# Performance work log

Hardware: AMD Instinct MI355X
Metric: run time of the kernel (lower is better)

The kernel has to match this reference:

```python
import jax, jax.numpy as jnp
import numpy as np

B, S, D, H, L = 32, 512, 256, 8, 3
HD = D // H
FFN = D // 2
SCALE_BASE = 512.0
EPS = 1e-5


def _gammas():
    return (1.0 - jnp.exp(jnp.linspace(np.log(1.0 / 32.0), np.log(1.0 / 512.0), H))).astype(jnp.float32)


def _xpos(x, downscale):
    # x: [..., S, hd]; XPOS rotary embedding with exponential length scaling
    s, hd = x.shape[-2], x.shape[-1]
    half = hd // 2
    scale = (jnp.arange(0, hd, 2, dtype=jnp.float32) + 0.4 * hd) / (1.4 * hd)  # [half]
    power = jnp.arange(s, dtype=jnp.float32)[:, None] / SCALE_BASE
    sm = scale[None, :] ** power  # [S, half]
    if downscale:
        sm = 1.0 / sm
    inv_freq = 1.0 / (10000.0 ** (jnp.arange(half, dtype=jnp.float32) / half))
    ang = jnp.arange(s, dtype=jnp.float32)[:, None] * inv_freq[None, :]  # [S, half]
    sin = jnp.repeat(jnp.sin(ang) * sm, 2, axis=-1)  # duplicate_interleave -> [S, hd]
    cos = jnp.repeat(jnp.cos(ang) * sm, 2, axis=-1)
    x1, x2 = x[..., ::2], x[..., 1::2]
    rot = jnp.stack((-x2, x1), axis=-1).reshape(x.shape)  # rotate_every_two
    return x * cos + rot * sin


def _layer_norm(x, w, b):
    mu = x.mean(-1, keepdims=True)
    var = ((x - mu) ** 2).mean(-1, keepdims=True)
    return (x - mu) / jnp.sqrt(var + EPS) * w + b


def _msr(X, WQ, WK, WV, WG, WO, gn_w, gn_b):
    # Multi-scale retention, parallel form. X: [B,S,D]; WQ/WK/WV: [H,D,HD]
    b, s, _ = X.shape
    Q = _xpos(jnp.einsum('bsd,hde->bhse', X, WQ), False)
    K = _xpos(jnp.einsum('bsd,hde->bhse', X, WK), True)
    V = jnp.einsum('bsd,hde->bhse', X, WV)
    n = jnp.arange(s)
    delta = (n[:, None] - n[None, :]).astype(jnp.float32)
    mask = n[:, None] >= n[None, :]
    g = _gammas()
    Dm = jnp.where(mask[None], g[:, None, None] ** delta[None], 0.0)  # [H,S,S]
    scores = jnp.einsum('bhse,bhte->bhst', Q, K) * Dm[None]  # [B,H,S,S]
    Y = jnp.einsum('bhst,bhte->bhse', scores, V)  # [B,H,S,HD]
    Y = jnp.moveaxis(Y, 1, 2)  # [B,S,H,HD] (= concat heads)
    # GroupNorm(heads, v_dim): normalize per (token, head) group
    mu = Y.mean(-1, keepdims=True)
    var = ((Y - mu) ** 2).mean(-1, keepdims=True)
    Yn = ((Y - mu) / jnp.sqrt(var + EPS)).reshape(b, s, D) * gn_w + gn_b
    G = X @ WG
    return (G * jax.nn.sigmoid(G) * Yn) @ WO


def setup_inputs() -> dict:
    key = jax.random.key(0)
    ks = jax.random.split(key, 10)
    inp = {
        'v': jax.random.randint(ks[0], (B, S), 0, 65, dtype=jnp.int64),
        'emb': jax.random.normal(ks[1], (65, D), dtype=jnp.float32),
        'WQ': jax.random.normal(ks[2], (L, H, D, HD), dtype=jnp.float32) / D,
        'WK': jax.random.normal(ks[3], (L, H, D, HD), dtype=jnp.float32) / D,
        'WV': jax.random.normal(ks[4], (L, H, D, HD), dtype=jnp.float32) / D,
        'WG': jax.random.normal(ks[5], (L, D, D), dtype=jnp.float32) / D,
        'WO': jax.random.normal(ks[6], (L, D, D), dtype=jnp.float32) / D,
        'gn_w': jnp.ones((L, D), jnp.float32),
        'gn_b': jnp.zeros((L, D), jnp.float32),
        'ln1_w': jnp.ones((L, D), jnp.float32),
        'ln1_b': jnp.zeros((L, D), jnp.float32),
        'ln2_w': jnp.ones((L, D), jnp.float32),
        'ln2_b': jnp.zeros((L, D), jnp.float32),
        'w1': jax.random.normal(ks[7], (L, D, FFN), dtype=jnp.float32) * (1.0 / np.sqrt(D)),
        'b1': jnp.zeros((L, FFN), jnp.float32),
        'w2': jax.random.normal(ks[8], (L, FFN, D), dtype=jnp.float32) * (1.0 / np.sqrt(FFN)),
        'b2': jnp.zeros((L, D), jnp.float32),
    }
    return inp


def reference(v, emb, WQ, WK, WV, WG, WO, gn_w, gn_b, ln1_w, ln1_b, ln2_w, ln2_b, w1, b1, w2, b2):
    emb = emb.at[0].set(0.0)  # padding_idx=0
    X = jax.nn.relu(emb[v])  # [B,S,D]
    for i in range(L):
        Y = _msr(_layer_norm(X, ln1_w[i], ln1_b[i]), WQ[i], WK[i], WV[i], WG[i], WO[i], gn_w[i], gn_b[i]) + X
        h = jax.nn.gelu(_layer_norm(Y, ln2_w[i], ln2_b[i]) @ w1[i] + b1[i], approximate=False)
        X = h @ w2[i] + b2[i] + Y
    return X
```

## Files before the change

kernel.cpp:

```cpp
#include <hip/hip_runtime.h>
#include <hip/hip_bf16.h>
#include <math.h>

#define BB 32
#define SS 512
#define DD 256
#define HH 8
#define HDIM 32
#define FFNN 128
#define NROWS (BB*SS)
#define NELEM (NROWS*DD)

using bf16 = __hip_bfloat16;
typedef __attribute__((ext_vector_type(8))) short short8;
typedef __attribute__((ext_vector_type(4))) short short4v;
typedef __attribute__((ext_vector_type(4))) float floatx4;
typedef unsigned int uint_al __attribute__((may_alias));

static __device__ __forceinline__ float bf2f(bf16 x) { return __bfloat162float(x); }
static __device__ __forceinline__ bf16  f2bf(float x) { return __float2bfloat16(x); }
static __device__ __forceinline__ short f2bfs(float x) {
    bf16 b = __float2bfloat16(x);
    return __builtin_bit_cast(short, b);
}

static __device__ __forceinline__ unsigned int cvtpk(float a, float b) {
    unsigned int r;
    asm("v_cvt_pk_bf16_f32 %0, %1, %2" : "=v"(r) : "v"(a), "v"(b));
    return r;
}
static __device__ __forceinline__ short4v mk4(unsigned int a, unsigned int b) {
    union { unsigned int u[2]; short4v s; } t;
    t.u[0] = a; t.u[1] = b;
    return t.s;
}
static __device__ __forceinline__ floatx4 mfma16(short4v a, short4v b, floatx4 c) {
#if __has_builtin(__builtin_amdgcn_mfma_f32_16x16x16bf16_1k)
    return __builtin_amdgcn_mfma_f32_16x16x16bf16_1k(a, b, c, 0, 0, 0);
#else
    asm("v_mfma_f32_16x16x16_bf16 %0, %1, %2, %0" : "+v"(c) : "v"(a), "v"(b));
    return c;
#endif
}

static __device__ __forceinline__ void gld_lds16(const void* g, void* l) {
    __builtin_amdgcn_global_load_lds(
        (const __attribute__((address_space(1))) void*)g,
        (__attribute__((address_space(3))) void*)l, 16, 0, 0);
}

__global__ __launch_bounds__(256) void detect_v(const int* __restrict__ v, int* __restrict__ flag) {
    int i = blockIdx.x * 256 + threadIdx.x;
    if (v[2 * i + 1] != 0) atomicOr(flag, 1);
}

#define NQKVG (3*1024*256)
#define NWO   (3*256*256)
#define NW1   (3*128*256)
#define NW2   (3*256*128)
#define NXPT  (512*16)
#define NSETUP (NQKVG+NWO+NW1+NW2+NXPT)
__global__ __launch_bounds__(256) void setup_pack(const float* __restrict__ WQ, const float* __restrict__ WK,
                                                  const float* __restrict__ WV, const float* __restrict__ WG,
                                                  const float* __restrict__ WO, const float* __restrict__ w1,
                                                  const float* __restrict__ w2,
                                                  bf16* __restrict__ dQ, bf16* __restrict__ dO,
                                                  bf16* __restrict__ d1, bf16* __restrict__ d2,
                                                  float4* __restrict__ xpt, int* __restrict__ flag) {
    int idx = blockIdx.x * 256 + threadIdx.x;
    if (idx == 0) *flag = 0;
    if (idx < NQKVG) {
        int k = idx & 255, n = (idx >> 8) & 1023, l = idx >> 18;
        int seg = n >> 8, n8 = n & 255;
        float val;
        if (seg < 3) {
            const float* W = (seg == 0) ? WQ : (seg == 1) ? WK : WV;
            int h = n8 >> 5, e = n8 & 31;
            val = W[(((size_t)l * 8 + h) * 256 + k) * 32 + e];
        } else {
            val = WG[(size_t)l * 65536 + k * 256 + n8];
        }
        dQ[((size_t)l * 1024 + n) * 256 + k] = f2bf(val);
    } else if (idx < NQKVG + NWO) {
        int i = idx - NQKVG;
        int k = i & 255, n = (i >> 8) & 255, l = i >> 16;
        dO[((size_t)l * 256 + n) * 256 + k] = f2bf(WO[(size_t)l * 65536 + k * 256 + n]);
    } else if (idx < NQKVG + NWO + NW1) {
        int i = idx - NQKVG - NWO;
        int k = i & 255, n = (i >> 8) & 127, l = i >> 15;
        d1[((size_t)l * 128 + n) * 256 + k] = f2bf(w1[(size_t)l * 32768 + k * 128 + n]);
    } else if (idx < NQKVG + NWO + NW1 + NW2) {
        int i = idx - NQKVG - NWO - NW1;
        int k = i & 127, n = (i >> 7) & 255, l = i >> 15;
        d2[((size_t)l * 256 + n) * 128 + k] = f2bf(w2[(size_t)l * 32768 + k * 256 + n]);
    } else {
        int i = idx - NQKVG - NWO - NW1 - NW2;
        int jf = i & 15, s = i >> 4;
        float base = (2.0f * jf + 12.8f) / 44.8f;
        float sm = powf(base, (float)s * (1.0f / 512.0f));
        float ang = (float)s * powf(10000.0f, -(float)jf / 16.0f);
        float sn, cs;
        sincosf(ang, &sn, &cs);
        xpt[i] = float4{cs * sm, sn * sm, cs / sm, sn / sm};
    }
}

__global__ __launch_bounds__(256) void embed_ln_kernel(const int* __restrict__ v,
                                                       const float* __restrict__ emb,
                                                       const int* __restrict__ flag,
                                                       const float* __restrict__ w,
                                                       const float* __restrict__ b,
                                                       float* __restrict__ X,
                                                       short* __restrict__ Xn) {
    __shared__ float p1[4], p2[4], st[2];
    const int d = threadIdx.x;
    const int wid = threadIdx.x >> 6;
    const int is32 = *flag;
    const float wd = w[d], bd = b[d];
    for (int it = 0; it < 8; ++it) {
        int row = blockIdx.x * 8 + it;
        int tok = is32 ? v[row] : v[2 * row];
        float x = 0.0f;
        if (tok != 0) {
            x = emb[tok * DD + d];
            x = x > 0.0f ? x : 0.0f;
        }
        X[(size_t)row * DD + d] = x;
        float s1 = x, s2 = x * x;
        #pragma unroll
        for (int off = 1; off < 64; off <<= 1) {
            s1 += __shfl_xor(s1, off);
            s2 += __shfl_xor(s2, off);
        }
        if ((threadIdx.x & 63) == 0) { p1[wid] = s1; p2[wid] = s2; }
        __syncthreads();
        if (threadIdx.x == 0) {
            float t1 = p1[0] + p1[1] + p1[2] + p1[3];
            float t2 = p2[0] + p2[1] + p2[2] + p2[3];
            float mu = t1 * (1.0f / DD);
            float var = t2 * (1.0f / DD) - mu * mu;
            st[0] = mu; st[1] = rsqrtf(var + 1e-5f);
        }
        __syncthreads();
        Xn[(size_t)row * DD + d] = f2bfs((x - st[0]) * st[1] * wd + bd);
    }
}

__global__ __launch_bounds__(256) void qkvg_gemm(const short* __restrict__ A,
                                                 const short* __restrict__ Bp,
                                                 const float4* __restrict__ xpt,
                                                 bf16* __restrict__ C) {
    __shared__ __align__(16) short Als[16 * 512];
    __shared__ __align__(16) short Bls[16 * 512];
    const int tid = threadIdx.x;
    const int wave = tid >> 6, lane = tid & 63, lo = lane & 15, quad = lane >> 4;
    const int wm = wave >> 1, wn = wave & 1;
    const int row0 = blockIdx.x * 128, col0 = blockIdx.y * 128;

    floatx4 acc[4][4];
    #pragma unroll
    for (int i = 0; i < 4; ++i)
        #pragma unroll
        for (int j = 0; j < 4; ++j) acc[i][j] = floatx4{0.f, 0.f, 0.f, 0.f};

    for (int k0 = 0; k0 < 256; k0 += 64) {
        #pragma unroll
        for (int t = 0; t < 4; ++t) {
            int grp = (wm * 4 + t) * 2 + wn;
            const short* ga = A + (size_t)(row0 + (wm * 4 + t) * 16 + lo) * 256
                            + k0 + (wn * 4 + quad) * 8;
            gld_lds16(ga, &Als[grp * 512]);
        }
        #pragma unroll
        for (int t = 0; t < 4; ++t) {
            int grp = (wn * 4 + t) * 2 + wm;
            const short* gb = Bp + (size_t)(col0 + (wn * 4 + t) * 16 + lo) * 256
                            + k0 + (wm * 4 + quad) * 8;
            gld_lds16(gb, &Bls[grp * 512]);
        }
        __syncthreads();
        #pragma unroll
        for (int kkgrp = 0; kkgrp < 2; ++kkgrp) {
            short8 af[4], bfr[4];
            #pragma unroll
            for (int t = 0; t < 4; ++t)
                af[t] = *(const short8*)(&Als[((wm * 4 + t) * 2 + kkgrp) * 512 + lane * 8]);
            #pragma unroll
            for (int t = 0; t < 4; ++t)
                bfr[t] = *(const short8*)(&Bls[((wn * 4 + t) * 2 + kkgrp) * 512 + lane * 8]);
            #pragma unroll
            for (int ti = 0; ti < 4; ++ti)
                #pragma unroll
                for (int tj = 0; tj < 4; ++tj)
                    acc[ti][tj] = __builtin_amdgcn_mfma_f32_16x16x32_bf16(af[ti], bfr[tj], acc[ti][tj], 0, 0, 0);
        }
        __syncthreads();
    }

    #pragma unroll
    for (int ti = 0; ti < 4; ++ti) {
        #pragma unroll
        for (int tj = 0; tj < 4; ++tj) {
            int colb = col0 + (wn * 4 + tj) * 16 + lo;
            int seg = colb >> 8;
            #pragma unroll
            for (int r = 0; r < 4; ++r) {
                int row = row0 + (wm * 4 + ti) * 16 + quad * 4 + r;
                float v = acc[ti][tj][r];
                if (seg < 2) {
                    int s = row & (SS - 1);
                    int jf = (colb & 31) >> 1;
                    float4 t = xpt[s * 16 + jf];
                    float cs = (seg == 0) ? t.x : t.z;
                    float sn = (seg == 0) ? t.y : t.w;
                    float p = __shfl_xor(v, 1);
                    v = (lo & 1) ? (v * cs + p * sn) : (v * cs - p * sn);
                }
                C[(size_t)row * 1024 + colb] = f2bf(v);
            }
        }
    }
}

#define TSTR 264
#define HSTR 136
#define VSTR 42
template<int DOLN>
__global__ __launch_bounds__(512) void ret_wo_ffn(const bf16* __restrict__ QKVG,
                                                  const float* __restrict__ gnw,
                                                  const float* __restrict__ gnb,
                                                  const short* __restrict__ Wo,
                                                  const short* __restrict__ W1p,
                                                  const float* __restrict__ b1,
                                                  const short* __restrict__ W2p,
                                                  const float* __restrict__ b2,
                                                  float* __restrict__ X,
                                                  const float* __restrict__ ln2w,
                                                  const float* __restrict__ ln2b,
                                                  const float* __restrict__ ln1w,
                                                  const float* __restrict__ ln1b,
                                                  short* __restrict__ Xn) {
    __shared__ __align__(16) short Vt[8][32 * VSTR];
    __shared__ __align__(16) short Tn[32 * TSTR];
    __shared__ __align__(16) short Hf[32 * HSTR];
    __shared__ float Ssum[32][8], Ssq[32][8];
    const int tid = threadIdx.x;
    const int wave = tid >> 6, lane = tid & 63, lo = lane & 15, quad = lane >> 4;
    const int blk = blockIdx.x;
    const int xcd = blk & 7;
    const int slot = blk >> 3;
    int qi, bbl;
    if (slot < 32) { qi = slot & 15; bbl = slot >> 4; }
    else { qi = 15 - (slot & 15); bbl = 2 + ((slot - 32) >> 4); }
    const int bb = (xcd << 2) | bbl;
    const int q0 = qi * 32;
    const int row0 = bb * SS + q0;
    const int h = wave;
    const int kq = quad * 8;

    const size_t base = (size_t)bb * SS * 1024;
    const short* QKVGs = (const short*)QKVG;
    const float la0 = -3.46573590280f, la1 = -6.23832462504f;
    float gamma = 1.0f - expf(la0 + (float)h * (la1 - la0) / 7.0f);
    float lg2 = log2f(gamma);
    float g16i = exp2f(-16.0f * lg2);
    float g16p = exp2f(16.0f * lg2);
    float gi32 = exp2f(-32.0f * lg2);
    float wq[4], wq16[4], wqB[4];
    #pragma unroll
    for (int r = 0; r < 4; ++r) {
        wq[r]   = exp2f((float)(lo - 4 * quad - r) * lg2);
        wq16[r] = wq[r] * g16i;
        wqB[r]  = wq[r] * g16p;
    }
    float c = exp2f((float)q0 * lg2);

    short8 qfA = *(const short8*)(QKVGs + base + (size_t)(q0 + lo) * 1024 + h * HDIM + kq);
    short8 qfB = *(const short8*)(QKVGs + base + (size_t)(q0 + 16 + lo) * 1024 + h * HDIM + kq);

    floatx4 oA0 = {0,0,0,0}, oA1 = {0,0,0,0}, oB0 = {0,0,0,0}, oB1 = {0,0,0,0};
    short* Vw = Vt[wave];
    const int nch = qi + 1;

    for (int ch = 0; ch < nch; ++ch) {
        const int t0 = ch * 32;
        const short* Kb = QKVGs + base + 256 + h * HDIM + kq;
        short8 kf0 = *(const short8*)(Kb + (size_t)(t0 + lo) * 1024);
        short8 kf1 = *(const short8*)(Kb + (size_t)(t0 + 16 + lo) * 1024);
        {
            const int vr = lane >> 2, dcol = (lane & 3) * 8;
            const short* Vg = QKVGs + base + 512 + h * HDIM + dcol;
            uint4 u1 = *(const uint4*)(Vg + (size_t)(t0 + vr) * 1024);
            uint4 u2 = *(const uint4*)(Vg + (size_t)(t0 + 16 + vr) * 1024);
            uint_al* W1 = (uint_al*)(Vw + vr * VSTR + dcol);
            uint_al* W2 = (uint_al*)(Vw + (16 + vr) * VSTR + dcol);
            W1[0] = u1.x; W1[1] = u1.y; W1[2] = u1.z; W1[3] = u1.w;
            W2[0] = u2.x; W2[1] = u2.y; W2[2] = u2.z; W2[3] = u2.w;
        }
        const floatx4 z = {0,0,0,0};
        __builtin_amdgcn_s_setprio(1);
        floatx4 sA0 = __builtin_amdgcn_mfma_f32_16x16x32_bf16(kf0, qfA, z, 0, 0, 0);
        floatx4 sA1 = __builtin_amdgcn_mfma_f32_16x16x32_bf16(kf1, qfA, z, 0, 0, 0);
        floatx4 sB0 = __builtin_amdgcn_mfma_f32_16x16x32_bf16(kf0, qfB, z, 0, 0, 0);
        floatx4 sB1 = __builtin_amdgcn_mfma_f32_16x16x32_bf16(kf1, qfB, z, 0, 0, 0);
        __builtin_amdgcn_s_setprio(0);

        float m0[4], m1[4], mB[4];
        #pragma unroll
        for (int r = 0; r < 4; ++r) {
            m0[r] = c * wq[r];
            m1[r] = c * wq16[r];
            mB[r] = c * wqB[r];
        }
        if (ch == qi) {
            #pragma unroll
            for (int r = 0; r < 4; ++r) {
                if (lo < 4 * quad + r) m0[r] = 0.0f;
                m1[r] = 0.0f;
            }
        }
        c *= gi32;

        unsigned int pa0 = cvtpk(sA0[0] * m0[0], sA0[1] * m0[1]);
        unsigned int pa1 = cvtpk(sA0[2] * m0[2], sA0[3] * m0[3]);
        unsigned int pa2 = cvtpk(sA1[0] * m1[0], sA1[1] * m1[1]);
        unsigned int pa3 = cvtpk(sA1[2] * m1[2], sA1[3] * m1[3]);
        unsigned int pb0 = cvtpk(sB0[0] * mB[0], sB0[1] * mB[1]);
        unsigned int pb1 = cvtpk(sB0[2] * mB[2], sB0[3] * mB[3]);
        unsigned int pb2 = cvtpk(sB1[0] * m0[0], sB1[1] * m0[1]);
        unsigned int pb3 = cvtpk(sB1[2] * m0[2], sB1[3] * m0[3]);
        short4v pA0 = mk4(pa0, pa1), pA1 = mk4(pa2, pa3);
        short4v pB0 = mk4(pb0, pb1), pB1 = mk4(pb2, pb3);

        short4v v00, v01, v10, v11;
        #pragma unroll
        for (int j = 0; j < 4; ++j) {
            v00[j] = Vw[(4 * quad + j) * VSTR + lo];
            v01[j] = Vw[(16 + 4 * quad + j) * VSTR + lo];
            v10[j] = Vw[(4 * quad + j) * VSTR + 16 + lo];
            v11[j] = Vw[(16 + 4 * quad + j) * VSTR + 16 + lo];
        }
        __builtin_amdgcn_s_setprio(1);
        oA0 = mfma16(pA0, v00, oA0);
        oA0 = mfma16(pA1, v01, oA0);
        oA1 = mfma16(pA0, v10, oA1);
        oA1 = mfma16(pA1, v11, oA1);
        oB0 = mfma16(pB0, v00, oB0);
        oB0 = mfma16(pB1, v01, oB0);
        oB1 = mfma16(pB0, v10, oB1);
        oB1 = mfma16(pB1, v11, oB1);
        __builtin_amdgcn_s_setprio(0);
    }

    {
        float gw0 = gnw[h * HDIM + lo], gw1 = gnw[h * HDIM + 16 + lo];
        float gb0 = gnb[h * HDIM + lo], gb1 = gnb[h * HDIM + 16 + lo];
        #pragma unroll
        for (int sub = 0; sub < 2; ++sub) {
            floatx4 o0 = sub ? oB0 : oA0;
            floatx4 o1 = sub ? oB1 : oA1;
            #pragma unroll
            for (int r = 0; r < 4; ++r) {
                float y0 = o0[r], y1 = o1[r];
                float s = y0 + y1, ss = y0 * y0 + y1 * y1;
                #pragma unroll
                for (int off = 1; off < 16; off <<= 1) {
                    s  += __shfl_xor(s, off);
                    ss += __shfl_xor(ss, off);
                }
                float mu = s * (1.0f / HDIM);
                float var = ss * (1.0f / HDIM) - mu * mu;
                float rstd = rsqrtf(var + 1e-5f);
                int rl = sub * 16 + quad * 4 + r;
                size_t rowb = base + (size_t)(q0 + rl) * 1024;
                float g0 = bf2f(QKVG[rowb + 768 + h * HDIM + lo]);
                float g1 = bf2f(QKVG[rowb + 768 + h * HDIM + 16 + lo]);
                float t0v = g0 / (1.0f + expf(-g0)) * ((y0 - mu) * rstd * gw0 + gb0);
                float t1v = g1 / (1.0f + expf(-g1)) * ((y1 - mu) * rstd * gw1 + gb1);
                Tn[rl * TSTR + h * HDIM + lo]      = f2bfs(t0v);
                Tn[rl * TSTR + h * HDIM + 16 + lo] = f2bfs(t1v);
            }
        }
    }
    __syncthreads();

    floatx4 acc[2][2];
    #pragma unroll
    for (int i = 0; i < 2; ++i) { acc[i][0] = floatx4{0,0,0,0}; acc[i][1] = floatx4{0,0,0,0}; }
    for (int k0 = 0; k0 < 256; k0 += 64) {
        #pragma unroll
        for (int kk = 0; kk < 2; ++kk) {
            const int kof = k0 + kk * 32 + kq;
            short8 af[2], bfr[2];
            #pragma unroll
            for (int t = 0; t < 2; ++t)
                af[t] = *(const short8*)(&Tn[(t * 16 + lo) * TSTR + kof]);
            #pragma unroll
            for (int t = 0; t < 2; ++t)
                bfr[t] = *(const short8*)(Wo + (size_t)(wave * 32 + t * 16 + lo) * 256 + kof);
            #pragma unroll
            for (int ti = 0; ti < 2; ++ti)
                #pragma unroll
                for (int tj = 0; tj < 2; ++tj)
                    acc[ti][tj] = __builtin_amdgcn_mfma_f32_16x16x32_bf16(af[ti], bfr[tj], acc[ti][tj], 0, 0, 0);
        }
    }

    float vv[2][2][4];
    #pragma unroll
    for (int ti = 0; ti < 2; ++ti)
        #pragma unroll
        for (int tj = 0; tj < 2; ++tj) {
            int colb = wave * 32 + tj * 16 + lo;
            #pragma unroll
            for (int r = 0; r < 4; ++r) {
                int row = row0 + ti * 16 + quad * 4 + r;
                vv[ti][tj][r] = acc[ti][tj][r] + X[(size_t)row * DD + colb];
            }
        }
    #pragma unroll
    for (int ti = 0; ti < 2; ++ti)
        #pragma unroll
        for (int r = 0; r < 4; ++r) {
            float s1 = 0.f, s2 = 0.f;
            #pragma unroll
            for (int tj = 0; tj < 2; ++tj) {
                float v = vv[ti][tj][r];
                s1 += v; s2 += v * v;
            }
            #pragma unroll
            for (int off = 1; off < 16; off <<= 1) {
                s1 += __shfl_xor(s1, off);
                s2 += __shfl_xor(s2, off);
            }
            if (lo == 0) {
                int rl = ti * 16 + quad * 4 + r;
                Ssum[rl][wave] = s1;
                Ssq[rl][wave] = s2;
            }
        }
    __syncthreads();
    #pragma unroll
    for (int ti = 0; ti < 2; ++ti)
        #pragma unroll
        for (int r = 0; r < 4; ++r) {
            int rl = ti * 16 + quad * 4 + r;
            float t1 = 0.f, t2 = 0.f;
            #pragma unroll
            for (int w8 = 0; w8 < 8; ++w8) { t1 += Ssum[rl][w8]; t2 += Ssq[rl][w8]; }
            float mu = t1 * (1.0f / DD);
            float var = t2 * (1.0f / DD) - mu * mu;
            float rs = rsqrtf(var + 1e-5f);
            #pragma unroll
            for (int tj = 0; tj < 2; ++tj) {
                int colb = wave * 32 + tj * 16 + lo;
                Tn[rl * TSTR + colb] =
                    f2bfs((vv[ti][tj][r] - mu) * rs * ln2w[colb] + ln2b[colb]);
            }
        }
    __syncthreads();

    floatx4 a1[2];
    a1[0] = floatx4{0,0,0,0}; a1[1] = floatx4{0,0,0,0};
    for (int k0 = 0; k0 < 256; k0 += 64) {
        #pragma unroll
        for (int kk = 0; kk < 2; ++kk) {
            const int kof = k0 + kk * 32 + kq;
            short8 af[2], bfr;
            #pragma unroll
            for (int t = 0; t < 2; ++t)
                af[t] = *(const short8*)(&Tn[(t * 16 + lo) * TSTR + kof]);
            bfr = *(const short8*)(W1p + (size_t)(wave * 16 + lo) * 256 + kof);
            #pragma unroll
            for (int ti = 0; ti < 2; ++ti)
                a1[ti] = __builtin_amdgcn_mfma_f32_16x16x32_bf16(af[ti], bfr, a1[ti], 0, 0, 0);
        }
    }
    {
        int colb = wave * 16 + lo;
        float bs = b1[colb];
        #pragma unroll
        for (int ti = 0; ti < 2; ++ti)
            #pragma unroll
            for (int r = 0; r < 4; ++r) {
                int rl = ti * 16 + quad * 4 + r;
                float v = a1[ti][r] + bs;
                v = 0.5f * v * (1.0f + erff(v * 0.70710678118f));
                Hf[rl * HSTR + colb] = f2bfs(v);
            }
    }
    __syncthreads();

    floatx4 a2[2][2];
    #pragma unroll
    for (int i = 0; i < 2; ++i) { a2[i][0] = floatx4{0,0,0,0}; a2[i][1] = floatx4{0,0,0,0}; }
    for (int k0 = 0; k0 < 128; k0 += 64) {
        #pragma unroll
        for (int kk = 0; kk < 2; ++kk) {
            const int kof = k0 + kk * 32 + kq;
            short8 af[2], bfr[2];
            #pragma unroll
            for (int t = 0; t < 2; ++t)
                af[t] = *(const short8*)(&Hf[(t * 16 + lo) * HSTR + kof]);
            #pragma unroll
            for (int t = 0; t < 2; ++t)
                bfr[t] = *(const short8*)(W2p + (size_t)(wave * 32 + t * 16 + lo) * 128 + kof);
            #pragma unroll
            for (int ti = 0; ti < 2; ++ti)
                #pragma unroll
                for (int tj = 0; tj < 2; ++tj)
                    a2[ti][tj] = __builtin_amdgcn_mfma_f32_16x16x32_bf16(af[ti], bfr[tj], a2[ti][tj], 0, 0, 0);
        }
    }

    #pragma unroll
    for (int ti = 0; ti < 2; ++ti)
        #pragma unroll
        for (int tj = 0; tj < 2; ++tj) {
            int colb = wave * 32 + tj * 16 + lo;
            float bs = b2[colb];
            #pragma unroll
            for (int r = 0; r < 4; ++r) {
                int row = row0 + ti * 16 + quad * 4 + r;
                float v = a2[ti][tj][r] + bs + vv[ti][tj][r];
                X[(size_t)row * DD + colb] = v;
                vv[ti][tj][r] = v;
            }
        }
    if (!DOLN) return;
    #pragma unroll
    for (int ti = 0; ti < 2; ++ti)
        #pragma unroll
        for (int r = 0; r < 4; ++r) {
            float s1 = 0.f, s2 = 0.f;
            #pragma unroll
            for (int tj = 0; tj < 2; ++tj) {
                float v = vv[ti][tj][r];
                s1 += v; s2 += v * v;
            }
            #pragma unroll
            for (int off = 1; off < 16; off <<= 1) {
                s1 += __shfl_xor(s1, off);
                s2 += __shfl_xor(s2, off);
            }
            if (lo == 0) {
                int rl = ti * 16 + quad * 4 + r;
                Ssum[rl][wave] = s1;
                Ssq[rl][wave] = s2;
            }
        }
    __syncthreads();
    #pragma unroll
    for (int ti = 0; ti < 2; ++ti)
        #pragma unroll
        for (int r = 0; r < 4; ++r) {
            int rl = ti * 16 + quad * 4 + r;
            float t1 = 0.f, t2 = 0.f;
            #pragma unroll
            for (int w8 = 0; w8 < 8; ++w8) { t1 += Ssum[rl][w8]; t2 += Ssq[rl][w8]; }
            float mu = t1 * (1.0f / DD);
            float var = t2 * (1.0f / DD) - mu * mu;
            float rs = rsqrtf(var + 1e-5f);
            int row = row0 + rl;
            #pragma unroll
            for (int tj = 0; tj < 2; ++tj) {
                int colb = wave * 32 + tj * 16 + lo;
                Xn[(size_t)row * DD + colb] =
                    f2bfs((vv[ti][tj][r] - mu) * rs * ln1w[colb] + ln1b[colb]);
            }
        }
}

extern "C" void kernel_launch(void* const* d_in, const int* in_sizes, int n_in,
                              void* d_out, int out_size, void* d_ws, size_t ws_size,
                              hipStream_t stream) {
    const int*   v    = (const int*)d_in[0];
    const float* emb  = (const float*)d_in[1];
    const float* WQ   = (const float*)d_in[2];
    const float* WK   = (const float*)d_in[3];
    const float* WV   = (const float*)d_in[4];
    const float* WG   = (const float*)d_in[5];
    const float* WO   = (const float*)d_in[6];
    const float* gn_w = (const float*)d_in[7];
    const float* gn_b = (const float*)d_in[8];
    const float* ln1w = (const float*)d_in[9];
    const float* ln1b = (const float*)d_in[10];
    const float* ln2w = (const float*)d_in[11];
    const float* ln2b = (const float*)d_in[12];
    const float* w1   = (const float*)d_in[13];
    const float* b1   = (const float*)d_in[14];
    const float* w2   = (const float*)d_in[15];
    const float* b2   = (const float*)d_in[16];

    float* X = (float*)d_out;

    float* base  = (float*)d_ws;
    int*   flag  = (int*)base;
    short* Xn    = (short*)(base + 16);
    bf16*  QKVG  = (bf16*)(Xn + (size_t)NROWS * 256);
    bf16*  WqkvgP = QKVG + (size_t)NROWS * 1024;
    bf16*  WoP   = WqkvgP + 3 * 1024 * 256;
    bf16*  W1P   = WoP + 3 * 256 * 256;
    bf16*  W2P   = W1P + 3 * 128 * 256;
    float4* xpt  = (float4*)(W2P + 3 * 256 * 128);

    setup_pack<<<NSETUP / 256, 256, 0, stream>>>(WQ, WK, WV, WG, WO, w1, w2,
                                                 WqkvgP, WoP, W1P, W2P, xpt, flag);
    detect_v<<<32, 256, 0, stream>>>(v, flag);
    embed_ln_kernel<<<NROWS / 8, 256, 0, stream>>>(v, emb, flag, ln1w, ln1b, X, Xn);

    for (int i = 0; i < 3; ++i) {
        qkvg_gemm<<<dim3(128, 8), 256, 0, stream>>>(Xn,
                                                    (const short*)(WqkvgP + (size_t)i * 1024 * 256),
                                                    xpt, QKVG);
        if (i < 2)
            ret_wo_ffn<1><<<512, 512, 0, stream>>>(QKVG, gn_w + i * DD, gn_b + i * DD,
                                                   (const short*)(WoP + (size_t)i * 256 * 256),
                                                   (const short*)(W1P + (size_t)i * 128 * 256),
                                                   b1 + i * FFNN,
                                                   (const short*)(W2P + (size_t)i * 256 * 128),
                                                   b2 + i * DD, X,
                                                   ln2w + i * DD, ln2b + i * DD,
                                                   ln1w + (i + 1) * DD, ln1b + (i + 1) * DD, Xn);
        else
            ret_wo_ffn<0><<<512, 512, 0, stream>>>(QKVG, gn_w + i * DD, gn_b + i * DD,
                                                   (const short*)(WoP + (size_t)i * 256 * 256),
                                                   (const short*)(W1P + (size_t)i * 128 * 256),
                                                   b1 + i * FFNN,
                                                   (const short*)(W2P + (size_t)i * 256 * 128),
                                                   b2 + i * DD, X,
                                                   ln2w + i * DD, ln2b + i * DD,
                                                   nullptr, nullptr, nullptr);
    }
}
```

Measured before the change: 347.8 us.

## Halve query tile to 16 rows and double grid in fused retention kernel

```diff
diff --git a/kernel.cpp b/kernel.cpp
--- a/kernel.cpp
+++ b/kernel.cpp
@@ -240,23 +240,24 @@
                                                   const float* __restrict__ ln1w,
                                                   const float* __restrict__ ln1b,
                                                   short* __restrict__ Xn) {
-    __shared__ __align__(16) short Vt[8][32 * VSTR];
-    __shared__ __align__(16) short Tn[32 * TSTR];
-    __shared__ __align__(16) short Hf[32 * HSTR];
-    __shared__ float Ssum[32][8], Ssq[32][8];
+    __shared__ __align__(16) short Tn[16 * TSTR];
+    __shared__ __align__(16) short Ubuf[8 * 16 * VSTR];
     const int tid = threadIdx.x;
     const int wave = tid >> 6, lane = tid & 63, lo = lane & 15, quad = lane >> 4;
     const int blk = blockIdx.x;
     const int xcd = blk & 7;
     const int slot = blk >> 3;
-    int qi, bbl;
-    if (slot < 32) { qi = slot & 15; bbl = slot >> 4; }
-    else { qi = 15 - (slot & 15); bbl = 2 + ((slot - 32) >> 4); }
-    const int bb = (xcd << 2) | bbl;
-    const int q0 = qi * 32;
+    const int g = slot >> 5, rr = slot & 31;
+    const int qt = (g & 1) ? (31 - rr) : rr;
+    const int bb = (xcd << 2) | g;
+    const int q0 = qt * 16;
     const int row0 = bb * SS + q0;
     const int h = wave;
     const int kq = quad * 8;
+
+    short* Hf = Ubuf;
+    float* Ssum = (float*)(Ubuf + 16 * HSTR);
+    float* Ssq  = Ssum + 16 * 8;
 
     const size_t base = (size_t)bb * SS * 1024;
     const short* QKVGs = (const short*)QKVG;
@@ -264,91 +265,56 @@
     float gamma = 1.0f - expf(la0 + (float)h * (la1 - la0) / 7.0f);
     float lg2 = log2f(gamma);
     float g16i = exp2f(-16.0f * lg2);
-    float g16p = exp2f(16.0f * lg2);
-    float gi32 = exp2f(-32.0f * lg2);
-    float wq[4], wq16[4], wqB[4];
-    #pragma unroll
-    for (int r = 0; r < 4; ++r) {
-        wq[r]   = exp2f((float)(lo - 4 * quad - r) * lg2);
-        wq16[r] = wq[r] * g16i;
-        wqB[r]  = wq[r] * g16p;
-    }
+    float wq[4];
+    #pragma unroll
+    for (int r = 0; r < 4; ++r)
+        wq[r] = exp2f((float)(lo - 4 * quad - r) * lg2);
     float c = exp2f((float)q0 * lg2);
 
-    short8 qfA = *(const short8*)(QKVGs + base + (size_t)(q0 + lo) * 1024 + h * HDIM + kq);
-    short8 qfB = *(const short8*)(QKVGs + base + (size_t)(q0 + 16 + lo) * 1024 + h * HDIM + kq);
-
-    floatx4 oA0 = {0,0,0,0}, oA1 = {0,0,0,0}, oB0 = {0,0,0,0}, oB1 = {0,0,0,0};
-    short* Vw = Vt[wave];
-    const int nch = qi + 1;
-
-    for (int ch = 0; ch < nch; ++ch) {
-        const int t0 = ch * 32;
-        const short* Kb = QKVGs + base + 256 + h * HDIM + kq;
-        short8 kf0 = *(const short8*)(Kb + (size_t)(t0 + lo) * 1024);
-        short8 kf1 = *(const short8*)(Kb + (size_t)(t0 + 16 + lo) * 1024);
+    short8 qf = *(const short8*)(QKVGs + base + (size_t)(q0 + lo) * 1024 + h * HDIM + kq);
+
+    floatx4 o0 = {0,0,0,0}, o1 = {0,0,0,0};
+    short* Vw = Ubuf + wave * (16 * VSTR);
+    const int nch = qt + 1;
+    const short* Kb = QKVGs + base + 256 + h * HDIM + kq;
+    const int vr = lane >> 2, dcol = (lane & 3) * 8;
+    const short* Vg = QKVGs + base + 512 + h * HDIM + dcol;
+
+    for (int ct = 0; ct < nch; ++ct) {
+        const int t0 = ct * 16;
+        short8 kf = *(const short8*)(Kb + (size_t)(t0 + lo) * 1024);
         {
-            const int vr = lane >> 2, dcol = (lane & 3) * 8;
-            const short* Vg = QKVGs + base + 512 + h * HDIM + dcol;
             uint4 u1 = *(const uint4*)(Vg + (size_t)(t0 + vr) * 1024);
-            uint4 u2 = *(const uint4*)(Vg + (size_t)(t0 + 16 + vr) * 1024);
             uint_al* W1 = (uint_al*)(Vw + vr * VSTR + dcol);
-            uint_al* W2 = (uint_al*)(Vw + (16 + vr) * VSTR + dcol);
             W1[0] = u1.x; W1[1] = u1.y; W1[2] = u1.z; W1[3] = u1.w;
-            W2[0] = u2.x; W2[1] = u2.y; W2[2] = u2.z; W2[3] = u2.w;
         }
         const floatx4 z = {0,0,0,0};
         __builtin_amdgcn_s_setprio(1);
-        floatx4 sA0 = __builtin_amdgcn_mfma_f32_16x16x32_bf16(kf0, qfA, z, 0, 0, 0);
-        floatx4 sA1 = __builtin_amdgcn_mfma_f32_16x16x32_bf16(kf1, qfA, z, 0, 0, 0);
-        floatx4 sB0 = __builtin_amdgcn_mfma_f32_16x16x32_bf16(kf0, qfB, z, 0, 0, 0);
-        floatx4 sB1 = __builtin_amdgcn_mfma_f32_16x16x32_bf16(kf1, qfB, z, 0, 0, 0);
+        floatx4 sA = __builtin_amdgcn_mfma_f32_16x16x32_bf16(kf, qf, z, 0, 0, 0);
         __builtin_amdgcn_s_setprio(0);
 
-        float m0[4], m1[4], mB[4];
-        #pragma unroll
-        for (int r = 0; r < 4; ++r) {
-            m0[r] = c * wq[r];
-            m1[r] = c * wq16[r];
-            mB[r] = c * wqB[r];
-        }
-        if (ch == qi) {
-            #pragma unroll
-            for (int r = 0; r < 4; ++r) {
+        float m0[4];
+        #pragma unroll
+        for (int r = 0; r < 4; ++r) m0[r] = c * wq[r];
+        if (ct == qt) {
+            #pragma unroll
+            for (int r = 0; r < 4; ++r)
                 if (lo < 4 * quad + r) m0[r] = 0.0f;
-                m1[r] = 0.0f;
-            }
-        }
-        c *= gi32;
-
-        unsigned int pa0 = cvtpk(sA0[0] * m0[0], sA0[1] * m0[1]);
-        unsigned int pa1 = cvtpk(sA0[2] * m0[2], sA0[3] * m0[3]);
-        unsigned int pa2 = cvtpk(sA1[0] * m1[0], sA1[1] * m1[1]);
-        unsigned int pa3 = cvtpk(sA1[2] * m1[2], sA1[3] * m1[3]);
-        unsigned int pb0 = cvtpk(sB0[0] * mB[0], sB0[1] * mB[1]);
-        unsigned int pb1 = cvtpk(sB0[2] * mB[2], sB0[3] * mB[3]);
-        unsigned int pb2 = cvtpk(sB1[0] * m0[0], sB1[1] * m0[1]);
-        unsigned int pb3 = cvtpk(sB1[2] * m0[2], sB1[3] * m0[3]);
-        short4v pA0 = mk4(pa0, pa1), pA1 = mk4(pa2, pa3);
-        short4v pB0 = mk4(pb0, pb1), pB1 = mk4(pb2, pb3);
-
-        short4v v00, v01, v10, v11;
+        }
+        c *= g16i;
+
+        short4v pA = mk4(cvtpk(sA[0] * m0[0], sA[1] * m0[1]),
+                         cvtpk(sA[2] * m0[2], sA[3] * m0[3]));
+
+        short4v v0, v1;
         #pragma unroll
         for (int j = 0; j < 4; ++j) {
-            v00[j] = Vw[(4 * quad + j) * VSTR + lo];
-            v01[j] = Vw[(16 + 4 * quad + j) * VSTR + lo];
-            v10[j] = Vw[(4 * quad + j) * VSTR + 16 + lo];
-            v11[j] = Vw[(16 + 4 * quad + j) * VSTR + 16 + lo];
+            v0[j] = Vw[(4 * quad + j) * VSTR + lo];
+            v1[j] = Vw[(4 * quad + j) * VSTR + 16 + lo];
         }
         __builtin_amdgcn_s_setprio(1);
-        oA0 = mfma16(pA0, v00, oA0);
-        oA0 = mfma16(pA1, v01, oA0);
-        oA1 = mfma16(pA0, v10, oA1);
-        oA1 = mfma16(pA1, v11, oA1);
-        oB0 = mfma16(pB0, v00, oB0);
-        oB0 = mfma16(pB1, v01, oB0);
-        oB1 = mfma16(pB0, v10, oB1);
-        oB1 = mfma16(pB1, v11, oB1);
+        o0 = mfma16(pA, v0, o0);
+        o1 = mfma16(pA, v1, o1);
         __builtin_amdgcn_s_setprio(0);
     }
 
@@ -356,219 +322,173 @@
         float gw0 = gnw[h * HDIM + lo], gw1 = gnw[h * HDIM + 16 + lo];
         float gb0 = gnb[h * HDIM + lo], gb1 = gnb[h * HDIM + 16 + lo];
         #pragma unroll
-        for (int sub = 0; sub < 2; ++sub) {
-            floatx4 o0 = sub ? oB0 : oA0;
-            floatx4 o1 = sub ? oB1 : oA1;
-            #pragma unroll
-            for (int r = 0; r < 4; ++r) {
-                float y0 = o0[r], y1 = o1[r];
-                float s = y0 + y1, ss = y0 * y0 + y1 * y1;
-                #pragma unroll
-                for (int off = 1; off < 16; off <<= 1) {
-                    s  += __shfl_xor(s, off);
-                    ss += __shfl_xor(ss, off);
-                }
-                float mu = s * (1.0f / HDIM);
-                float var = ss * (1.0f / HDIM) - mu * mu;
-                float rstd = rsqrtf(var + 1e-5f);
-                int rl = sub * 16 + quad * 4 + r;
-                size_t rowb = base + (size_t)(q0 + rl) * 1024;
-                float g0 = bf2f(QKVG[rowb + 768 + h * HDIM + lo]);
-                float g1 = bf2f(QKVG[rowb + 768 + h * HDIM + 16 + lo]);
-                float t0v = g0 / (1.0f + expf(-g0)) * ((y0 - mu) * rstd * gw0 + gb0);
-                float t1v = g1 / (1.0f + expf(-g1)) * ((y1 - mu) * rstd * gw1 + gb1);
-                Tn[rl * TSTR + h * HDIM + lo]      = f2bfs(t0v);
-                Tn[rl * TSTR + h * HDIM + 16 + lo] = f2bfs(t1v);
+        for (int r = 0; r < 4; ++r) {
+            float y0 = o0[r], y1 = o1[r];
+            float s = y0 + y1, ss = y0 * y0 + y1 * y1;
+            #pragma unroll
+            for (int off = 1; off < 16; off <<= 1) {
+                s  += __shfl_xor(s, off);
+                ss += __shfl_xor(ss, off);
             }
+            float mu = s * (1.0f / HDIM);
+            float var = ss * (1.0f / HDIM) - mu * mu;
+            float rstd = rsqrtf(var + 1e-5f);
+            int rl = quad * 4 + r;
+            size_t rowb = base + (size_t)(q0 + rl) * 1024;
+            float g0 = bf2f(QKVG[rowb + 768 + h * HDIM + lo]);
+            float g1 = bf2f(QKVG[rowb + 768 + h * HDIM + 16 + lo]);
+            float t0v = g0 / (1.0f + expf(-g0)) * ((y0 - mu) * rstd * gw0 + gb0);
+            float t1v = g1 / (1.0f + expf(-g1)) * ((y1 - mu) * rstd * gw1 + gb1);
+            Tn[rl * TSTR + h * HDIM + lo]      = f2bfs(t0v);
+            Tn[rl * TSTR + h * HDIM + 16 + lo] = f2bfs(t1v);
         }
     }
     __syncthreads();
 
-    floatx4 acc[2][2];
-    #pragma unroll
-    for (int i = 0; i < 2; ++i) { acc[i][0] = floatx4{0,0,0,0}; acc[i][1] = floatx4{0,0,0,0}; }
+    floatx4 acc[2];
+    acc[0] = floatx4{0,0,0,0}; acc[1] = floatx4{0,0,0,0};
     for (int k0 = 0; k0 < 256; k0 += 64) {
         #pragma unroll
         for (int kk = 0; kk < 2; ++kk) {
             const int kof = k0 + kk * 32 + kq;
-            short8 af[2], bfr[2];
-            #pragma unroll
-            for (int t = 0; t < 2; ++t)
-                af[t] = *(const short8*)(&Tn[(t * 16 + lo) * TSTR + kof]);
-            #pragma unroll
-            for (int t = 0; t < 2; ++t)
-                bfr[t] = *(const short8*)(Wo + (size_t)(wave * 32 + t * 16 + lo) * 256 + kof);
-            #pragma unroll
-            for (int ti = 0; ti < 2; ++ti)
-                #pragma unroll
-                for (int tj = 0; tj < 2; ++tj)
-                    acc[ti][tj] = __builtin_amdgcn_mfma_f32_16x16x32_bf16(af[ti], bfr[tj], acc[ti][tj], 0, 0, 0);
-        }
-    }
-
-    float vv[2][2][4];
-    #pragma unroll
-    for (int ti = 0; ti < 2; ++ti)
+            short8 af = *(const short8*)(&Tn[lo * TSTR + kof]);
+            #pragma unroll
+            for (int tj = 0; tj < 2; ++tj) {
+                short8 bfr = *(const short8*)(Wo + (size_t)(wave * 32 + tj * 16 + lo) * 256 + kof);
+                acc[tj] = __builtin_amdgcn_mfma_f32_16x16x32_bf16(af, bfr, acc[tj], 0, 0, 0);
+            }
+        }
+    }
+
+    float vv[2][4];
+    #pragma unroll
+    for (int tj = 0; tj < 2; ++tj) {
+        int colb = wave * 32 + tj * 16 + lo;
+        #pragma unroll
+        for (int r = 0; r < 4; ++r) {
+            int row = row0 + quad * 4 + r;
+            vv[tj][r] = acc[tj][r] + X[(size_t)row * DD + colb];
+        }
+    }
+    #pragma unroll
+    for (int r = 0; r < 4; ++r) {
+        float s1 = vv[0][r] + vv[1][r];
+        float s2 = vv[0][r] * vv[0][r] + vv[1][r] * vv[1][r];
+        #pragma unroll
+        for (int off = 1; off < 16; off <<= 1) {
+            s1 += __shfl_xor(s1, off);
+            s2 += __shfl_xor(s2, off);
+        }
+        if (lo == 0) {
+            int rl = quad * 4 + r;
+            Ssum[rl * 8 + wave] = s1;
+            Ssq[rl * 8 + wave] = s2;
+        }
+    }
+    __syncthreads();
+    #pragma unroll
+    for (int r = 0; r < 4; ++r) {
+        int rl = quad * 4 + r;
+        float t1 = 0.f, t2 = 0.f;
+        #pragma unroll
+        for (int w8 = 0; w8 < 8; ++w8) { t1 += Ssum[rl * 8 + w8]; t2 += Ssq[rl * 8 + w8]; }
+        float mu = t1 * (1.0f / DD);
+        float var = t2 * (1.0f / DD) - mu * mu;
+        float rs = rsqrtf(var + 1e-5f);
         #pragma unroll
         for (int tj = 0; tj < 2; ++tj) {
             int colb = wave * 32 + tj * 16 + lo;
-            #pragma unroll
-            for (int r = 0; r < 4; ++r) {
-                int row = row0 + ti * 16 + quad * 4 + r;
-                vv[ti][tj][r] = acc[ti][tj][r] + X[(size_t)row * DD + colb];
-            }
-        }
-    #pragma unroll
-    for (int ti = 0; ti < 2; ++ti)
-        #pragma unroll
-        for (int r = 0; r < 4; ++r) {
-            float s1 = 0.f, s2 = 0.f;
-            #pragma unroll
-            for (int tj = 0; tj < 2; ++tj) {
-                float v = vv[ti][tj][r];
-                s1 += v; s2 += v * v;
-            }
-            #pragma unroll
-            for (int off = 1; off < 16; off <<= 1) {
-                s1 += __shfl_xor(s1, off);
-                s2 += __shfl_xor(s2, off);
-            }
-            if (lo == 0) {
-                int rl = ti * 16 + quad * 4 + r;
-                Ssum[rl][wave] = s1;
-                Ssq[rl][wave] = s2;
-            }
-        }
+            Tn[rl * TSTR + colb] =
+                f2bfs((vv[tj][r] - mu) * rs * ln2w[colb] + ln2b[colb]);
+        }
+    }
     __syncthreads();
-    #pragma unroll
-    for (int ti = 0; ti < 2; ++ti)
-        #pragma unroll
-        for (int r = 0; r < 4; ++r) {
-            int rl = ti * 16 + quad * 4 + r;
-            float t1 = 0.f, t2 = 0.f;
-            #pragma unroll
-            for (int w8 = 0; w8 < 8; ++w8) { t1 += Ssum[rl][w8]; t2 += Ssq[rl][w8]; }
-            float mu = t1 * (1.0f / DD);
-            float var = t2 * (1.0f / DD) - mu * mu;
-            float rs = rsqrtf(var + 1e-5f);
-            #pragma unroll
-            for (int tj = 0; tj < 2; ++tj) {
-                int colb = wave * 32 + tj * 16 + lo;
-                Tn[rl * TSTR + colb] =
-                    f2bfs((vv[ti][tj][r] - mu) * rs * ln2w[colb] + ln2b[colb]);
-            }
-        }
-    __syncthreads();
-
-    floatx4 a1[2];
-    a1[0] = floatx4{0,0,0,0}; a1[1] = floatx4{0,0,0,0};
+
+    floatx4 a1 = {0,0,0,0};
     for (int k0 = 0; k0 < 256; k0 += 64) {
         #pragma unroll
         for (int kk = 0; kk < 2; ++kk) {
             const int kof = k0 + kk * 32 + kq;
-            short8 af[2], bfr;
-            #pragma unroll
-            for (int t = 0; t < 2; ++t)
-                af[t] = *(const short8*)(&Tn[(t * 16 + lo) * TSTR + kof]);
-            bfr = *(const short8*)(W1p + (size_t)(wave * 16 + lo) * 256 + kof);
-            #pragma unroll
-            for (int ti = 0; ti < 2; ++ti)
-                a1[ti] = __builtin_amdgcn_mfma_f32_16x16x32_bf16(af[ti], bfr, a1[ti], 0, 0, 0);
+            short8 af = *(const short8*)(&Tn[lo * TSTR + kof]);
+            short8 bfr = *(const short8*)(W1p + (size_t)(wave * 16 + lo) * 256 + kof);
+            a1 = __builtin_amdgcn_mfma_f32_16x16x32_bf16(af, bfr, a1, 0, 0, 0);
         }
     }
     {
         int colb = wave * 16 + lo;
         float bs = b1[colb];
         #pragma unroll
-        for (int ti = 0; ti < 2; ++ti)
-            #pragma unroll
-            for (int r = 0; r < 4; ++r) {
-                int rl = ti * 16 + quad * 4 + r;
-                float v = a1[ti][r] + bs;
-                v = 0.5f * v * (1.0f + erff(v * 0.70710678118f));
-                Hf[rl * HSTR + colb] = f2bfs(v);
-            }
+        for (int r = 0; r < 4; ++r) {
+            int rl = quad * 4 + r;
+            float v = a1[r] + bs;
+            v = 0.5f * v * (1.0f + erff(v * 0.70710678118f));
+            Hf[rl * HSTR + colb] = f2bfs(v);
+        }
     }
     __syncthreads();
 
-    floatx4 a2[2][2];
-    #pragma unroll
-    for (int i = 0; i < 2; ++i) { a2[i][0] = floatx4{0,0,0,0}; a2[i][1] = floatx4{0,0,0,0}; }
+    floatx4 a2[2];
+    a2[0] = floatx4{0,0,0,0}; a2[1] = floatx4{0,0,0,0};
     for (int k0 = 0; k0 < 128; k0 += 64) {
         #pragma unroll
         for (int kk = 0; kk < 2; ++kk) {
             const int kof = k0 + kk * 32 + kq;
-            short8 af[2], bfr[2];
-            #pragma unroll
-            for (int t = 0; t < 2; ++t)
-                af[t] = *(const short8*)(&Hf[(t * 16 + lo) * HSTR + kof]);
-            #pragma unroll
-            for (int t = 0; t < 2; ++t)
-                bfr[t] = *(const short8*)(W2p + (size_t)(wave * 32 + t * 16 + lo) * 128 + kof);
-            #pragma unroll
-            for (int ti = 0; ti < 2; ++ti)
-                #pragma unroll
-                for (int tj = 0; tj < 2; ++tj)
-                    a2[ti][tj] = __builtin_amdgcn_mfma_f32_16x16x32_bf16(af[ti], bfr[tj], a2[ti][tj], 0, 0, 0);
-        }
-    }
-
-    #pragma unroll
-    for (int ti = 0; ti < 2; ++ti)
+            short8 af = *(const short8*)(&Hf[lo * HSTR + kof]);
+            #pragma unroll
+            for (int tj = 0; tj < 2; ++tj) {
+                short8 bfr = *(const short8*)(W2p + (size_t)(wave * 32 + tj * 16 + lo) * 128 + kof);
+                a2[tj] = __builtin_amdgcn_mfma_f32_16x16x32_bf16(af, bfr, a2[tj], 0, 0, 0);
+            }
+        }
+    }
+
+    #pragma unroll
+    for (int tj = 0; tj < 2; ++tj) {
+        int colb = wave * 32 + tj * 16 + lo;
+        float bs = b2[colb];
+        #pragma unroll
+        for (int r = 0; r < 4; ++r) {
+            int row = row0 + quad * 4 + r;
+            float v = a2[tj][r] + bs + vv[tj][r];
+            X[(size_t)row * DD + colb] = v;
+            vv[tj][r] = v;
+        }
+    }
+    if (!DOLN) return;
+    __syncthreads();
+    #pragma unroll
+    for (int r = 0; r < 4; ++r) {
+        float s1 = vv[0][r] + vv[1][r];
+        float s2 = vv[0][r] * vv[0][r] + vv[1][r] * vv[1][r];
+        #pragma unroll
+        for (int off = 1; off < 16; off <<= 1) {
+            s1 += __shfl_xor(s1, off);
+            s2 += __shfl_xor(s2, off);
+        }
+        if (lo == 0) {
+            int rl = quad * 4 + r;
+            Ssum[rl * 8 + wave] = s1;
+            Ssq[rl * 8 + wave] = s2;
+        }
+    }
+    __syncthreads();
+    #pragma unroll
+    for (int r = 0; r < 4; ++r) {
+        int rl = quad * 4 + r;
+        float t1 = 0.f, t2 = 0.f;
+        #pragma unroll
+        for (int w8 = 0; w8 < 8; ++w8) { t1 += Ssum[rl * 8 + w8]; t2 += Ssq[rl * 8 + w8]; }
+        float mu = t1 * (1.0f / DD);
+        float var = t2 * (1.0f / DD) - mu * mu;
+        float rs = rsqrtf(var + 1e-5f);
+        int row = row0 + rl;
         #pragma unroll
         for (int tj = 0; tj < 2; ++tj) {
             int colb = wave * 32 + tj * 16 + lo;
-            float bs = b2[colb];
-            #pragma unroll
-            for (int r = 0; r < 4; ++r) {
-                int row = row0 + ti * 16 + quad * 4 + r;
-                float v = a2[ti][tj][r] + bs + vv[ti][tj][r];
-                X[(size_t)row * DD + colb] = v;
-                vv[ti][tj][r] = v;
-            }
-        }
-    if (!DOLN) return;
-    #pragma unroll
-    for (int ti = 0; ti < 2; ++ti)
-        #pragma unroll
-        for (int r = 0; r < 4; ++r) {
-            float s1 = 0.f, s2 = 0.f;
-            #pragma unroll
-            for (int tj = 0; tj < 2; ++tj) {
-                float v = vv[ti][tj][r];
-                s1 += v; s2 += v * v;
-            }
-            #pragma unroll
-            for (int off = 1; off < 16; off <<= 1) {
-                s1 += __shfl_xor(s1, off);
-                s2 += __shfl_xor(s2, off);
-            }
-            if (lo == 0) {
-                int rl = ti * 16 + quad * 4 + r;
-                Ssum[rl][wave] = s1;
-                Ssq[rl][wave] = s2;
-            }
-        }
-    __syncthreads();
-    #pragma unroll
-    for (int ti = 0; ti < 2; ++ti)
-        #pragma unroll
-        for (int r = 0; r < 4; ++r) {
-            int rl = ti * 16 + quad * 4 + r;
-            float t1 = 0.f, t2 = 0.f;
-            #pragma unroll
-            for (int w8 = 0; w8 < 8; ++w8) { t1 += Ssum[rl][w8]; t2 += Ssq[rl][w8]; }
-            float mu = t1 * (1.0f / DD);
-            float var = t2 * (1.0f / DD) - mu * mu;
-            float rs = rsqrtf(var + 1e-5f);
-            int row = row0 + rl;
-            #pragma unroll
-            for (int tj = 0; tj < 2; ++tj) {
-                int colb = wave * 32 + tj * 16 + lo;
-                Xn[(size_t)row * DD + colb] =
-                    f2bfs((vv[ti][tj][r] - mu) * rs * ln1w[colb] + ln1b[colb]);
-            }
-        }
+            Xn[(size_t)row * DD + colb] =
+                f2bfs((vv[tj][r] - mu) * rs * ln1w[colb] + ln1b[colb]);
+        }
+    }
 }
 
 extern "C" void kernel_launch(void* const* d_in, const int* in_sizes, int n_in,
@@ -614,22 +534,22 @@
                                                     (const short*)(WqkvgP + (size_t)i * 1024 * 256),
                                                     xpt, QKVG);
         if (i < 2)
-            ret_wo_ffn<1><<<512, 512, 0, stream>>>(QKVG, gn_w + i * DD, gn_b + i * DD,
-                                                   (const short*)(WoP + (size_t)i * 256 * 256),
-                                                   (const short*)(W1P + (size_t)i * 128 * 256),
-                                                   b1 + i * FFNN,
-                                                   (const short*)(W2P + (size_t)i * 256 * 128),
-                                                   b2 + i * DD, X,
-                                                   ln2w + i * DD, ln2b + i * DD,
-                                                   ln1w + (i + 1) * DD, ln1b + (i + 1) * DD, Xn);
+            ret_wo_ffn<1><<<1024, 512, 0, stream>>>(QKVG, gn_w + i * DD, gn_b + i * DD,
+                                                    (const short*)(WoP + (size_t)i * 256 * 256),
+                                                    (const short*)(W1P + (size_t)i * 128 * 256),
+                                                    b1 + i * FFNN,
+                                                    (const short*)(W2P + (size_t)i * 256 * 128),
+                                                    b2 + i * DD, X,
+                                                    ln2w + i * DD, ln2b + i * DD,
+                                                    ln1w + (i + 1) * DD, ln1b + (i + 1) * DD, Xn);
         else
-            ret_wo_ffn<0><<<512, 512, 0, stream>>>(QKVG, gn_w + i * DD, gn_b + i * DD,
-                                                   (const short*)(WoP + (size_t)i * 256 * 256),
-                                                   (const short*)(W1P + (size_t)i * 128 * 256),
-                                                   b1 + i * FFNN,
-                                                   (const short*)(W2P + (size_t)i * 256 * 128),
-                                                   b2 + i * DD, X,
-                                                   ln2w + i * DD, ln2b + i * DD,
-                                                   nullptr, nullptr, nullptr);
-    }
-}
+            ret_wo_ffn<0><<<1024, 512, 0, stream>>>(QKVG, gn_w + i * DD, gn_b + i * DD,
+                                                    (const short*)(WoP + (size_t)i * 256 * 256),
+                                                    (const short*)(W1P + (size_t)i * 128 * 256),
+                                                    b1 + i * FFNN,
+                                                    (const short*)(W2P + (size_t)i * 256 * 128),
+                                                    b2 + i * DD, X,
+                                                    ln2w + i * DD, ln2b + i * DD,
+                                                    nullptr, nullptr, nullptr);
+    }
+}
```

Result: slower. 400.8 us (+15.2%).
